# Kernel tuning notes

Hardware: AMD Instinct MI355X
Metric: run time of the kernel (lower is better)

Reference implementation:

```python
import jax, jax.numpy as jnp
import numpy as np

K = 20
BN_INV = float(1.0 / np.sqrt(1.0 + 1e-5))  # BatchNorm eval with running_mean=0, running_var=1


def _leaky(h):
    return jnp.where(h >= 0, h, 0.2 * h)


def _knn_idx(x, k):
    # x: [B, C, N]; pairwise_distance = -(||xi||^2 + ||xj||^2 - 2 xi.xj); topk = nearest
    inner = jnp.einsum('bcn,bcm->bnm', x, x)
    xx = jnp.sum(x * x, axis=1)  # [B, N]
    pd = 2.0 * inner - xx[:, :, None] - xx[:, None, :]
    return jax.lax.top_k(pd, k)[1]  # [B, N, k]


def _edge_conv(x, w, g, b, k):
    # x: [B, C, N]; w: [Cout, 2C]
    idx = _knn_idx(x, k)
    xt = jnp.transpose(x, (0, 2, 1))  # [B, N, C]
    nb = jax.vmap(lambda f, i: f[i])(xt, idx)  # [B, N, k, C] gathered neighbors
    ctr = xt[:, :, None, :]
    feat = jnp.concatenate([nb - ctr, jnp.broadcast_to(ctr, nb.shape)], axis=-1)  # [B,N,k,2C]
    h = jnp.einsum('bnkc,oc->bnko', feat, w)
    h = _leaky(g * h * BN_INV + b)
    h = jnp.max(h, axis=2)  # max over k neighbors -> [B, N, Cout]
    return jnp.transpose(h, (0, 2, 1))  # [B, Cout, N]


def setup_inputs() -> dict:
    key = jax.random.key(0)
    ks = jax.random.split(key, 32)
    s = 0.05

    def w(i, shape):
        return jax.random.normal(ks[i], shape, dtype=jnp.float32) * s

    def gb(i, c):
        return (1.0 + 0.1 * jax.random.normal(ks[i], (c,), dtype=jnp.float32),
                0.1 * jax.random.normal(jax.random.fold_in(ks[i], 1), (c,), dtype=jnp.float32))

    g1, b1 = gb(1, 64); g2, b2 = gb(2, 64); g3, b3 = gb(3, 128); g4, b4 = gb(4, 256)
    gc, bc = gb(5, 1024); gf1, bf1 = gb(6, 512); gf2, bf2 = gb(7, 256)
    return {
        'x': jax.random.normal(ks[0], (8, 3, 2048), dtype=jnp.float32),
        'w1': w(8, (64, 6)),   'g1': g1, 'b1': b1,
        'w2': w(9, (64, 128)), 'g2': g2, 'b2': b2,
        'w3': w(10, (128, 128)), 'g3': g3, 'b3': b3,
        'w4': w(11, (256, 256)), 'g4': g4, 'b4': b4,
        'wc': w(12, (1024, 512)), 'gc': gc, 'bc': bc,
        'wf1': w(13, (512, 2048)), 'gf1': gf1, 'bf1': bf1,
        'wf2': w(14, (256, 512)), 'bwf2': w(15, (256,)), 'gf2': gf2, 'bf2': bf2,
        'wf3': w(16, (40, 256)), 'bwf3': w(17, (40,)),
    }


def reference(x, w1, g1, b1, w2, g2, b2, w3, g3, b3, w4, g4, b4,
              wc, gc, bc, wf1, gf1, bf1, wf2, bwf2, gf2, bf2, wf3, bwf3):
    x1 = _edge_conv(x, w1, g1, b1, K)   # [B, 64, N]
    x2 = _edge_conv(x1, w2, g2, b2, K)  # [B, 64, N]
    x3 = _edge_conv(x2, w3, g3, b3, K)  # [B, 128, N]
    x4 = _edge_conv(x3, w4, g4, b4, K)  # [B, 256, N]
    h = jnp.concatenate([x1, x2, x3, x4], axis=1)  # [B, 512, N]
    h = jnp.einsum('bcn,oc->bon', h, wc)
    h = _leaky(gc[:, None] * h * BN_INV + bc[:, None])  # [B, 1024, N]
    x5 = jnp.max(h, axis=2)
    x6 = jnp.mean(h, axis=2)
    h = jnp.concatenate([x5, x6], axis=1)  # [B, 2048]
    h = _leaky(gf1 * (h @ wf1.T) * BN_INV + bf1)   # fc1 (no bias) + BN + LeakyReLU
    h = _leaky(gf2 * (h @ wf2.T + bwf2) * BN_INV + bf2)  # fc2 + BN + LeakyReLU (dropout=eval identity)
    return h @ wf3.T + bwf3  # [B, numClass]
```

## Files before the change

kernel.cpp:

```cpp
#include <hip/hip_runtime.h>
#include <hip/hip_bf16.h>
#include <float.h>

#define BB 8
#define NN 2048
#define KK 20

static constexpr float BN_INV_F = 0.9999950000374997f;

typedef __attribute__((ext_vector_type(4))) float f32x4;
typedef __attribute__((ext_vector_type(8))) short s16x8;

__device__ __forceinline__ unsigned short f2bf(float f) {
    __hip_bfloat16 h = __float2bfloat16(f);
    return __builtin_bit_cast(unsigned short, h);
}
__device__ __forceinline__ float bf2f(unsigned short u) {
    unsigned int v = ((unsigned int)u) << 16;
    return __builtin_bit_cast(float, v);
}
__device__ __forceinline__ unsigned mono(float f) {
    unsigned b = __builtin_bit_cast(unsigned, f);
    return b ^ (unsigned)(((int)b >> 31) | 0x80000000);
}

__global__ void split_kernel(const float* __restrict__ w, unsigned short* __restrict__ hi,
                             unsigned short* __restrict__ lo, int n) {
    int t = blockIdx.x * blockDim.x + threadIdx.x;
    if (t >= n) return;
    float v = w[t];
    unsigned short h = f2bf(v);
    hi[t] = h;
    lo[t] = f2bf(v - bf2f(h));
}

__global__ void sqnorm_kernel(const float* __restrict__ x, float* __restrict__ xx, int C) {
    int t = blockIdx.x * blockDim.x + threadIdx.x;
    if (t >= BB * NN) return;
    int b = t / NN, n = t % NN;
    const float* xb = x + (size_t)b * C * NN + n;
    float s = 0.f;
    for (int c = 0; c < C; ++c) {
        float v = xb[(size_t)c * NN];
        s += v * v;
    }
    xx[t] = s;
}

__global__ __launch_bounds__(256, 4) void pd_kernel(const float* __restrict__ x,
                                                    const float* __restrict__ xx,
                                                    float* __restrict__ pd,
                                                    int C, int baseB) {
    __shared__ float ctrT[128][8];
    __shared__ float xns[8];

    int blk = blockIdx.x;
    int chalf = blk & 1;
    int rt = (blk >> 1) & 255;
    int b2 = blk >> 9;
    int b = baseB + b2;
    int rbase = rt * 8;
    int tid = threadIdx.x;
    const float* xb = x + (size_t)b * C * NN;

    for (int i = tid; i < C * 8; i += 256) {
        int c = i >> 3, r = i & 7;
        ctrT[c][r] = xb[(size_t)c * NN + rbase + r];
    }
    if (tid < 8) xns[tid] = xx[b * NN + rbase + tid];
    __syncthreads();

    int m0 = chalf * 1024 + tid * 4;
    float acc[8][4];
    #pragma unroll
    for (int r = 0; r < 8; ++r)
        #pragma unroll
        for (int j = 0; j < 4; ++j) acc[r][j] = 0.f;

    f32x4 xv = *(const f32x4*)(xb + m0);
    for (int c = 0; c + 1 < C; ++c) {
        f32x4 nxt = *(const f32x4*)(xb + (size_t)(c + 1) * NN + m0);
        f32x4 c0 = *(const f32x4*)&ctrT[c][0];
        f32x4 c1 = *(const f32x4*)&ctrT[c][4];
        #pragma unroll
        for (int j = 0; j < 4; ++j) {
            acc[0][j] += c0.x * xv[j]; acc[1][j] += c0.y * xv[j];
            acc[2][j] += c0.z * xv[j]; acc[3][j] += c0.w * xv[j];
            acc[4][j] += c1.x * xv[j]; acc[5][j] += c1.y * xv[j];
            acc[6][j] += c1.z * xv[j]; acc[7][j] += c1.w * xv[j];
        }
        xv = nxt;
    }
    {
        f32x4 c0 = *(const f32x4*)&ctrT[C - 1][0];
        f32x4 c1 = *(const f32x4*)&ctrT[C - 1][4];
        #pragma unroll
        for (int j = 0; j < 4; ++j) {
            acc[0][j] += c0.x * xv[j]; acc[1][j] += c0.y * xv[j];
            acc[2][j] += c0.z * xv[j]; acc[3][j] += c0.w * xv[j];
            acc[4][j] += c1.x * xv[j]; acc[5][j] += c1.y * xv[j];
            acc[6][j] += c1.z * xv[j]; acc[7][j] += c1.w * xv[j];
        }
    }
    f32x4 xm = *(const f32x4*)(xx + (size_t)b * NN + m0);
    #pragma unroll
    for (int r = 0; r < 8; ++r) {
        f32x4 out;
        #pragma unroll
        for (int j = 0; j < 4; ++j)
            out[j] = 2.f * acc[r][j] - xns[r] - xm[j];
        *(f32x4*)&pd[((size_t)(b2 * NN + rbase + r)) * NN + m0] = out;
    }
}

__global__ __launch_bounds__(256, 4) void topk_kernel(const float* __restrict__ pd,
                                                      int* __restrict__ idxout, int baseB) {
    __shared__ unsigned long long cand[4][128];
    int w = threadIdx.x >> 6, lane = threadIdx.x & 63;
    int rowc = blockIdx.x * 4 + w;
    const float* prow = pd + (size_t)rowc * NN;

    float fv[32];
    #pragma unroll
    for (int j4 = 0; j4 < 8; ++j4) {
        f32x4 v = *(const f32x4*)(prow + j4 * 256 + lane * 4);
        #pragma unroll
        for (int e = 0; e < 4; ++e) fv[j4 * 4 + e] = v[e];
    }

    float lm = fv[0];
    #pragma unroll
    for (int i = 1; i < 32; ++i) lm = fmaxf(lm, fv[i]);

    float v = lm;
    #pragma unroll
    for (int k = 2; k <= 64; k <<= 1)
        #pragma unroll
        for (int j = k >> 1; j > 0; j >>= 1) {
            float o = __shfl_xor(v, j, 64);
            bool up = ((lane & k) == 0);
            bool keepMax = up ? ((lane & j) == 0) : ((lane & j) != 0);
            float mx = fmaxf(v, o), mn = fminf(v, o);
            v = keepMax ? mx : mn;
        }
    float Tf = __shfl(v, KK - 1, 64);

    cand[w][lane] = 0ull;
    cand[w][64 + lane] = 0ull;
    __builtin_amdgcn_wave_barrier();
    int base = 0;
    #pragma unroll
    for (int i = 0; i < 32; ++i) {
        int col = (i >> 2) * 256 + lane * 4 + (i & 3);
        bool c = fv[i] >= Tf;
        unsigned long long mask = __ballot(c);
        if (c) {
            int pos = base + (int)__popcll(mask & ((1ull << lane) - 1ull));
            if (pos < 128)
                cand[w][pos] = ((unsigned long long)mono(fv[i]) << 32) | (unsigned)~col;
        }
        base += (int)__popcll(mask);
    }
    __builtin_amdgcn_wave_barrier();

    unsigned long long ka = cand[w][lane];
    auto cmpx = [&](unsigned long long& key, int j, bool up) {
        unsigned long long o = __shfl_xor(key, j, 64);
        bool keepMax = up ? ((lane & j) == 0) : ((lane & j) != 0);
        bool gt = key > o;
        unsigned long long mx = gt ? key : o, mn = gt ? o : key;
        key = keepMax ? mx : mn;
    };
    if (base <= 64) {
        #pragma unroll
        for (int k = 2; k <= 64; k <<= 1)
            #pragma unroll
            for (int j = k >> 1; j > 0; j >>= 1)
                cmpx(ka, j, (lane & k) == 0);
    } else {
        unsigned long long kb = cand[w][64 + lane];
        #pragma unroll
        for (int k = 2; k <= 128; k <<= 1) {
            #pragma unroll
            for (int j = k >> 1; j > 0; j >>= 1) {
                if (j == 64) {
                    unsigned long long mx = ka > kb ? ka : kb;
                    unsigned long long mn = ka > kb ? kb : ka;
                    ka = mx; kb = mn;
                } else {
                    bool upA, upB;
                    if (k == 128)     { upA = true; upB = true; }
                    else if (k == 64) { upA = true; upB = false; }
                    else              { upA = ((lane & k) == 0); upB = upA; }
                    cmpx(ka, j, upA);
                    cmpx(kb, j, upB);
                }
            }
        }
    }

    if (lane < KK) {
        int col = (int)~(unsigned)(ka & 0xFFFFFFFFull);
        int b = baseB + (rowc >> 11);
        int n = rowc & 2047;
        idxout[((size_t)(b * NN + n)) * KK + lane] = col;
    }
}

__global__ __launch_bounds__(256) void pq_gemm_kernel(const float* __restrict__ x,
                                                      const float* __restrict__ w,
                                                      float* __restrict__ Pt, float* __restrict__ Qt,
                                                      int C, int Cout) {
    __shared__ float wPT[128][8];
    __shared__ float wQT[128][8];
    int blk = blockIdx.x;
    int pass = blk & 1;
    int rest = blk >> 1;
    int nog = Cout >> 3;
    int b = rest / nog;
    int obase = (rest % nog) * 8;
    int tid = threadIdx.x;
    const float* xb = x + (size_t)b * C * NN;

    for (int i = tid; i < C * 8; i += 256) {
        int c = i >> 3, r = i & 7;
        wPT[c][r] = w[(size_t)(obase + r) * 2 * C + c];
        wQT[c][r] = w[(size_t)(obase + r) * 2 * C + C + c];
    }
    __syncthreads();

    int m0 = pass * 1024 + tid * 4;
    float aP[8][4], aQ[8][4];
    #pragma unroll
    for (int r = 0; r < 8; ++r)
        #pragma unroll
        for (int j = 0; j < 4; ++j) { aP[r][j] = 0.f; aQ[r][j] = 0.f; }

    for (int c = 0; c < C; ++c) {
        f32x4 xv = *(const f32x4*)(xb + (size_t)c * NN + m0);
        f32x4 p0 = *(const f32x4*)&wPT[c][0];
        f32x4 p1 = *(const f32x4*)&wPT[c][4];
        f32x4 q0 = *(const f32x4*)&wQT[c][0];
        f32x4 q1 = *(const f32x4*)&wQT[c][4];
        #pragma unroll
        for (int j = 0; j < 4; ++j) {
            aP[0][j] += p0.x * xv[j]; aP[1][j] += p0.y * xv[j];
            aP[2][j] += p0.z * xv[j]; aP[3][j] += p0.w * xv[j];
            aP[4][j] += p1.x * xv[j]; aP[5][j] += p1.y * xv[j];
            aP[6][j] += p1.z * xv[j]; aP[7][j] += p1.w * xv[j];
            aQ[0][j] += q0.x * xv[j]; aQ[1][j] += q0.y * xv[j];
            aQ[2][j] += q0.z * xv[j]; aQ[3][j] += q0.w * xv[j];
            aQ[4][j] += q1.x * xv[j]; aQ[5][j] += q1.y * xv[j];
            aQ[6][j] += q1.z * xv[j]; aQ[7][j] += q1.w * xv[j];
        }
    }
    #pragma unroll
    for (int j = 0; j < 4; ++j) {
        size_t base = ((size_t)b * NN + m0 + j) * Cout + obase;
        f32x4 vP0, vP1, vQ0, vQ1;
        #pragma unroll
        for (int r = 0; r < 4; ++r) { vP0[r] = aP[r][j]; vP1[r] = aP[r + 4][j];
                                      vQ0[r] = aQ[r][j]; vQ1[r] = aQ[r + 4][j]; }
        *(f32x4*)&Pt[base] = vP0; *(f32x4*)&Pt[base + 4] = vP1;
        *(f32x4*)&Qt[base] = vQ0; *(f32x4*)&Qt[base + 4] = vQ1;
    }
}

__global__ __launch_bounds__(256) void edge_max_kernel(const float* __restrict__ Pt,
                                                       const float* __restrict__ Qt,
                                                       const int* __restrict__ idx,
                                                       const float* __restrict__ g,
                                                       const float* __restrict__ bt,
                                                       float* __restrict__ xf32,
                                                       unsigned short* __restrict__ Fhi,
                                                       unsigned short* __restrict__ Flo,
                                                       int coff, int Cout) {
    __shared__ int lidx[16][KK];
    int lanesPerN = Cout >> 2;
    int npw = 64 / lanesPerN;
    int nPerBlock = 4 * npw;

    int blk = blockIdx.x;
    int b = blk / (NN / nPerBlock);
    int nbase = (blk % (NN / nPerBlock)) * nPerBlock;
    int tid = threadIdx.x, wid = tid >> 6, lane = tid & 63;

    for (int i = tid; i < nPerBlock * KK; i += 256) {
        int ln = i / KK, k = i % KK;
        lidx[ln][k] = idx[((size_t)(b * NN + nbase + ln)) * KK + k];
    }
    __syncthreads();

    int nsub = lane / lanesPerN;
    int ol = (lane & (lanesPerN - 1)) * 4;
    int nrow = wid * npw + nsub;
    int n = nbase + nrow;

    const float* Pb = Pt + (size_t)b * NN * Cout;
    size_t rowbase = (size_t)n * Cout + ol;
    f32x4 Pn = *(const f32x4*)&Pb[rowbase];
    f32x4 Qn = *(const f32x4*)(Qt + (size_t)b * NN * Cout + rowbase);
    f32x4 off4 = Qn - Pn;
    f32x4 sc4 = *(const f32x4*)&g[ol];
    f32x4 bs4 = *(const f32x4*)&bt[ol];
    #pragma unroll
    for (int e = 0; e < 4; ++e) sc4[e] *= BN_INV_F;

    f32x4 mx4 = { -FLT_MAX, -FLT_MAX, -FLT_MAX, -FLT_MAX };
    #pragma unroll 4
    for (int k = 0; k < KK; ++k) {
        int m = lidx[nrow][k];
        f32x4 pv = *(const f32x4*)&Pb[(size_t)m * Cout + ol];
        #pragma unroll
        for (int e = 0; e < 4; ++e) {
            float y = sc4[e] * (pv[e] + off4[e]) + bs4[e];
            y = (y >= 0.f) ? y : 0.2f * y;
            mx4[e] = fmaxf(mx4[e], y);
        }
    }

    if (xf32) {
        #pragma unroll
        for (int e = 0; e < 4; ++e)
            xf32[((size_t)b * Cout + ol + e) * NN + n] = mx4[e];
    }
    size_t fb = ((size_t)b * NN + n) * 512 + coff + ol;
    ushort4 h4, l4;
    #pragma unroll
    for (int e = 0; e < 4; ++e) {
        unsigned short h = f2bf(mx4[e]);
        ((unsigned short*)&h4)[e] = h;
        ((unsigned short*)&l4)[e] = f2bf(mx4[e] - bf2f(h));
    }
    *(ushort4*)&Fhi[fb] = h4;
    *(ushort4*)&Flo[fb] = l4;
}

__global__ __launch_bounds__(256) void conv_mfma_kernel(const unsigned short* __restrict__ Whi,
                                                        const unsigned short* __restrict__ Wlo,
                                                        const unsigned short* __restrict__ Fhi,
                                                        const unsigned short* __restrict__ Flo,
                                                        const float* __restrict__ gc,
                                                        const float* __restrict__ bc,
                                                        float* __restrict__ pmax,
                                                        float* __restrict__ psum) {
    __shared__ unsigned short As[128 * 64] __attribute__((aligned(16)));
    __shared__ unsigned short Bs[128 * 64] __attribute__((aligned(16)));

    int blk = blockIdx.x;
    int nt = blk & 15, ot = (blk >> 4) & 7, b = blk >> 7;
    int obase = ot * 128, nbase = nt * 128;
    int tid = threadIdx.x, lane = tid & 63, wid = tid >> 6;
    int wo = wid >> 1, wn = wid & 1;

    f32x4 acc[4][4];
    #pragma unroll
    for (int m = 0; m < 4; ++m)
        #pragma unroll
        for (int q = 0; q < 4; ++q) acc[m][q] = (f32x4){0.f, 0.f, 0.f, 0.f};

    int srow = tid >> 1, sb = (tid & 1) * 4;

    for (int kt = 0; kt < 24; ++kt) {
        int seg = kt >> 3;
        int kc = (kt & 7) * 64;
        const unsigned short* Asrc = ((seg == 2) ? Wlo : Whi) + (size_t)obase * 512 + kc;
        const unsigned short* Bsrc = ((seg == 1) ? Flo : Fhi) + ((size_t)b * NN + nbase) * 512 + kc;
        __syncthreads();
        #pragma unroll
        for (int s = 0; s < 4; ++s) {
            int slot = sb + s;
            uint4 av = *(const uint4*)(Asrc + (size_t)srow * 512 + slot * 8);
            *(uint4*)(As + srow * 64 + ((slot ^ (srow & 7)) * 8)) = av;
            uint4 bv = *(const uint4*)(Bsrc + (size_t)srow * 512 + slot * 8);
            *(uint4*)(Bs + srow * 64 + ((slot ^ (srow & 7)) * 8)) = bv;
        }
        __syncthreads();
        #pragma unroll
        for (int ks = 0; ks < 2; ++ks) {
            s16x8 af[4], bf[4];
            #pragma unroll
            for (int m = 0; m < 4; ++m) {
                int r = wo * 64 + m * 16 + (lane & 15);
                int slot = (ks * 4 + (lane >> 4)) ^ (r & 7);
                af[m] = *(const s16x8*)(As + r * 64 + slot * 8);
                int r2 = wn * 64 + m * 16 + (lane & 15);
                int slot2 = (ks * 4 + (lane >> 4)) ^ (r2 & 7);
                bf[m] = *(const s16x8*)(Bs + r2 * 64 + slot2 * 8);
            }
            #pragma unroll
            for (int m = 0; m < 4; ++m)
                #pragma unroll
                for (int q = 0; q < 4; ++q)
                    acc[m][q] = __builtin_amdgcn_mfma_f32_16x16x32_bf16(af[m], bf[q], acc[m][q], 0, 0, 0);
        }
    }

    __syncthreads();
    float* redm = (float*)As;
    float* reds = redm + 256;
    #pragma unroll
    for (int m = 0; m < 4; ++m) {
        #pragma unroll
        for (int rg = 0; rg < 4; ++rg) {
            int olocal = wo * 64 + m * 16 + (lane >> 4) * 4 + rg;
            int o = obase + olocal;
            float scv = gc[o] * BN_INV_F, bsv = bc[o];
            float mx = -FLT_MAX, sm = 0.f;
            #pragma unroll
            for (int q = 0; q < 4; ++q) {
                float y = scv * acc[m][q][rg] + bsv;
                y = (y >= 0.f) ? y : 0.2f * y;
                mx = fmaxf(mx, y);
                sm += y;
            }
            #pragma unroll
            for (int d = 1; d < 16; d <<= 1) {
                mx = fmaxf(mx, __shfl_xor(mx, d, 64));
                sm += __shfl_xor(sm, d, 64);
            }
            if ((lane & 15) == 0) {
                redm[wn * 128 + olocal] = mx;
                reds[wn * 128 + olocal] = sm;
            }
        }
    }
    __syncthreads();
    if (tid < 128) {
        float mx = fmaxf(redm[tid], redm[128 + tid]);
        float sm = reds[tid] + reds[128 + tid];
        size_t base = ((size_t)b * 1024 + obase + tid) * 16 + nt;
        pmax[base] = mx;
        psum[base] = sm;
    }
}

__global__ void pool_reduce_kernel(const float* __restrict__ pmax, const float* __restrict__ psum,
                                   float* __restrict__ x56) {
    int t = blockIdx.x * blockDim.x + threadIdx.x;
    if (t >= BB * 1024) return;
    int b = t >> 10, o = t & 1023;
    float mx = -FLT_MAX, sm = 0.f;
    for (int ch = 0; ch < 16; ++ch) {
        mx = fmaxf(mx, pmax[(size_t)t * 16 + ch]);
        sm += psum[(size_t)t * 16 + ch];
    }
    x56[(size_t)b * 2048 + o] = mx;
    x56[(size_t)b * 2048 + 1024 + o] = sm * (1.0f / 2048.0f);
}

__global__ void fc_kernel(const float* __restrict__ in, const float* __restrict__ w,
                          const float* __restrict__ bw, const float* __restrict__ g,
                          const float* __restrict__ bt, float* __restrict__ out,
                          int Cin, int Cout, int mode) {
    int gt = blockIdx.x * blockDim.x + threadIdx.x;
    int wid = gt >> 6;
    int lane = threadIdx.x & 63;
    if (wid >= BB * Cout) return;
    int b = wid / Cout, o = wid % Cout;
    const float* ib = in + (size_t)b * Cin;
    const float* wr = w + (size_t)o * Cin;
    float acc = 0.f;
    for (int c = lane; c < Cin; c += 64) acc += ib[c] * wr[c];
    for (int d = 32; d >= 1; d >>= 1) acc += __shfl_down(acc, d, 64);
    if (lane == 0) {
        float y;
        if (mode == 0)      { y = g[o] * acc * BN_INV_F + bt[o]; y = (y >= 0.f) ? y : 0.2f * y; }
        else if (mode == 1) { float h = acc + bw[o]; y = g[o] * h * BN_INV_F + bt[o]; y = (y >= 0.f) ? y : 0.2f * y; }
        else                { y = acc + bw[o]; }
        out[(size_t)b * Cout + o] = y;
    }
}

extern "C" void kernel_launch(void* const* d_in, const int* in_sizes, int n_in,
                              void* d_out, int out_size, void* d_ws, size_t ws_size,
                              hipStream_t stream) {
    const float* x    = (const float*)d_in[0];
    const float* w1   = (const float*)d_in[1];
    const float* g1   = (const float*)d_in[2];
    const float* b1   = (const float*)d_in[3];
    const float* w2   = (const float*)d_in[4];
    const float* g2   = (const float*)d_in[5];
    const float* b2   = (const float*)d_in[6];
    const float* w3   = (const float*)d_in[7];
    const float* g3   = (const float*)d_in[8];
    const float* b3   = (const float*)d_in[9];
    const float* w4   = (const float*)d_in[10];
    const float* g4   = (const float*)d_in[11];
    const float* b4   = (const float*)d_in[12];
    const float* wc   = (const float*)d_in[13];
    const float* gc   = (const float*)d_in[14];
    const float* bc   = (const float*)d_in[15];
    const float* wf1  = (const float*)d_in[16];
    const float* gf1  = (const float*)d_in[17];
    const float* bf1  = (const float*)d_in[18];
    const float* wf2  = (const float*)d_in[19];
    const float* bwf2 = (const float*)d_in[20];
    const float* gf2  = (const float*)d_in[21];
    const float* bf2  = (const float*)d_in[22];
    const float* wf3  = (const float*)d_in[23];
    const float* bwf3 = (const float*)d_in[24];

    char* ws = (char*)d_ws;
    size_t off = 0;
    auto alloc = [&](size_t nbytes) {
        char* p = ws + off;
        off += (nbytes + 255) & ~(size_t)255;
        return p;
    };
    float* xx   = (float*)alloc((size_t)BB * NN * 4);
    int*   idx  = (int*)  alloc((size_t)BB * NN * KK * 4);
    float* Pt   = (float*)alloc((size_t)BB * NN * 256 * 4);
    float* Qt   = (float*)alloc((size_t)BB * NN * 256 * 4);
    float* x1   = (float*)alloc((size_t)BB * 64 * NN * 4);
    float* x2   = (float*)alloc((size_t)BB * 64 * NN * 4);
    float* x3   = (float*)alloc((size_t)BB * 128 * NN * 4);
    unsigned short* Fhi = (unsigned short*)alloc((size_t)BB * NN * 512 * 2);
    unsigned short* Flo = (unsigned short*)alloc((size_t)BB * NN * 512 * 2);
    unsigned short* Whi = (unsigned short*)alloc((size_t)1024 * 512 * 2);
    unsigned short* Wlo = (unsigned short*)alloc((size_t)1024 * 512 * 2);
    float* pmax = (float*)alloc((size_t)BB * 1024 * 16 * 4);
    float* psum = (float*)alloc((size_t)BB * 1024 * 16 * 4);
    float* x56  = (float*)alloc((size_t)BB * 2048 * 4);
    float* f1   = (float*)alloc((size_t)BB * 512 * 4);
    float* f2   = (float*)alloc((size_t)BB * 256 * 4);

    float* pdbuf = Pt;

    split_kernel<<<(1024 * 512 + 255) / 256, 256, 0, stream>>>(wc, Whi, Wlo, 1024 * 512);

    struct Layer { const float* xin; int C; const float* w; const float* g; const float* bt;
                   float* xout; int Cout; int coff; };
    Layer L[4] = {
        { x,  3,   w1, g1, b1, x1,      64,  0   },
        { x1, 64,  w2, g2, b2, x2,      64,  64  },
        { x2, 64,  w3, g3, b3, x3,      128, 128 },
        { x3, 128, w4, g4, b4, nullptr, 256, 256 },
    };

    for (int l = 0; l < 4; ++l) {
        sqnorm_kernel<<<(BB * NN) / 256, 256, 0, stream>>>(L[l].xin, xx, L[l].C);
        for (int ch = 0; ch < 4; ++ch) {
            pd_kernel<<<1024, 256, 0, stream>>>(L[l].xin, xx, pdbuf, L[l].C, ch * 2);
            topk_kernel<<<1024, 256, 0, stream>>>(pdbuf, idx, ch * 2);
        }
        pq_gemm_kernel<<<BB * (L[l].Cout / 8) * 2, 256, 0, stream>>>(L[l].xin, L[l].w, Pt, Qt, L[l].C, L[l].Cout);
        int nPerBlock = 4 * (64 / (L[l].Cout >> 2));
        edge_max_kernel<<<BB * (NN / nPerBlock), 256, 0, stream>>>(Pt, Qt, idx, L[l].g, L[l].bt,
                                                                   L[l].xout, Fhi, Flo, L[l].coff, L[l].Cout);
    }

    conv_mfma_kernel<<<BB * 8 * 16, 256, 0, stream>>>(Whi, Wlo, Fhi, Flo, gc, bc, pmax, psum);
    pool_reduce_kernel<<<(BB * 1024 + 255) / 256, 256, 0, stream>>>(pmax, psum, x56);
    fc_kernel<<<(BB * 512 * 64 + 255) / 256, 256, 0, stream>>>(x56, wf1, nullptr, gf1, bf1, f1, 2048, 512, 0);
    fc_kernel<<<(BB * 256 * 64 + 255) / 256, 256, 0, stream>>>(f1, wf2, bwf2, gf2, bf2, f2, 512, 256, 1);
    fc_kernel<<<(BB * 40 * 64 + 255) / 256, 256, 0, stream>>>(f2, wf3, bwf3, nullptr, nullptr, (float*)d_out, 256, 40, 2);
}
```

Measured before the change: 849.9 us.

## Fuse pairwise-distance and top-k into one kernel using shared-memory rows

Replaces the chunked pd_kernel + topk_kernel pairs with a single kernel per layer that computes the distance rows for 4 points at a time into LDS and then selects the top-k directly from shared memory. This removes the global write and re-read of the full distance matrix and cuts eight launches per layer down to one. In exchange, each block handles 8 rows in two batches of 4 with extra syncthreads. It also needs about 36KB of LDS per block, which may limit occupancy, and the smaller 4-row register tile re-reads x for each batch.

```diff
diff --git a/kernel.cpp b/kernel.cpp
--- a/kernel.cpp
+++ b/kernel.cpp
@@ -47,163 +47,163 @@
     xx[t] = s;
 }
 
-__global__ __launch_bounds__(256, 4) void pd_kernel(const float* __restrict__ x,
-                                                    const float* __restrict__ xx,
-                                                    float* __restrict__ pd,
-                                                    int C, int baseB) {
-    __shared__ float ctrT[128][8];
+__global__ __launch_bounds__(256, 4) void knn_fused_kernel(const float* __restrict__ x,
+                                                           const float* __restrict__ xx,
+                                                           int* __restrict__ idxout, int C) {
+    __shared__ float pdl[4][NN];
+    __shared__ char ubuf[4096];
     __shared__ float xns[8];
 
+    float* ctrT = (float*)ubuf;
+    unsigned long long (*cand)[128] = (unsigned long long (*)[128])ubuf;
+
     int blk = blockIdx.x;
-    int chalf = blk & 1;
-    int rt = (blk >> 1) & 255;
-    int b2 = blk >> 9;
-    int b = baseB + b2;
-    int rbase = rt * 8;
+    int b = blk / (NN / 8);
+    int rbase = (blk % (NN / 8)) * 8;
     int tid = threadIdx.x;
     const float* xb = x + (size_t)b * C * NN;
 
-    for (int i = tid; i < C * 8; i += 256) {
-        int c = i >> 3, r = i & 7;
-        ctrT[c][r] = xb[(size_t)c * NN + rbase + r];
-    }
     if (tid < 8) xns[tid] = xx[b * NN + rbase + tid];
-    __syncthreads();
-
-    int m0 = chalf * 1024 + tid * 4;
-    float acc[8][4];
-    #pragma unroll
-    for (int r = 0; r < 8; ++r)
-        #pragma unroll
-        for (int j = 0; j < 4; ++j) acc[r][j] = 0.f;
-
-    f32x4 xv = *(const f32x4*)(xb + m0);
-    for (int c = 0; c + 1 < C; ++c) {
-        f32x4 nxt = *(const f32x4*)(xb + (size_t)(c + 1) * NN + m0);
-        f32x4 c0 = *(const f32x4*)&ctrT[c][0];
-        f32x4 c1 = *(const f32x4*)&ctrT[c][4];
-        #pragma unroll
-        for (int j = 0; j < 4; ++j) {
-            acc[0][j] += c0.x * xv[j]; acc[1][j] += c0.y * xv[j];
-            acc[2][j] += c0.z * xv[j]; acc[3][j] += c0.w * xv[j];
-            acc[4][j] += c1.x * xv[j]; acc[5][j] += c1.y * xv[j];
-            acc[6][j] += c1.z * xv[j]; acc[7][j] += c1.w * xv[j];
-        }
-        xv = nxt;
-    }
-    {
-        f32x4 c0 = *(const f32x4*)&ctrT[C - 1][0];
-        f32x4 c1 = *(const f32x4*)&ctrT[C - 1][4];
-        #pragma unroll
-        for (int j = 0; j < 4; ++j) {
-            acc[0][j] += c0.x * xv[j]; acc[1][j] += c0.y * xv[j];
-            acc[2][j] += c0.z * xv[j]; acc[3][j] += c0.w * xv[j];
-            acc[4][j] += c1.x * xv[j]; acc[5][j] += c1.y * xv[j];
-            acc[6][j] += c1.z * xv[j]; acc[7][j] += c1.w * xv[j];
-        }
-    }
-    f32x4 xm = *(const f32x4*)(xx + (size_t)b * NN + m0);
-    #pragma unroll
-    for (int r = 0; r < 8; ++r) {
-        f32x4 out;
-        #pragma unroll
-        for (int j = 0; j < 4; ++j)
-            out[j] = 2.f * acc[r][j] - xns[r] - xm[j];
-        *(f32x4*)&pd[((size_t)(b2 * NN + rbase + r)) * NN + m0] = out;
-    }
-}
-
-__global__ __launch_bounds__(256, 4) void topk_kernel(const float* __restrict__ pd,
-                                                      int* __restrict__ idxout, int baseB) {
-    __shared__ unsigned long long cand[4][128];
-    int w = threadIdx.x >> 6, lane = threadIdx.x & 63;
-    int rowc = blockIdx.x * 4 + w;
-    const float* prow = pd + (size_t)rowc * NN;
-
-    float fv[32];
-    #pragma unroll
-    for (int j4 = 0; j4 < 8; ++j4) {
-        f32x4 v = *(const f32x4*)(prow + j4 * 256 + lane * 4);
-        #pragma unroll
-        for (int e = 0; e < 4; ++e) fv[j4 * 4 + e] = v[e];
-    }
-
-    float lm = fv[0];
-    #pragma unroll
-    for (int i = 1; i < 32; ++i) lm = fmaxf(lm, fv[i]);
-
-    float v = lm;
-    #pragma unroll
-    for (int k = 2; k <= 64; k <<= 1)
-        #pragma unroll
-        for (int j = k >> 1; j > 0; j >>= 1) {
-            float o = __shfl_xor(v, j, 64);
-            bool up = ((lane & k) == 0);
-            bool keepMax = up ? ((lane & j) == 0) : ((lane & j) != 0);
-            float mx = fmaxf(v, o), mn = fminf(v, o);
-            v = keepMax ? mx : mn;
-        }
-    float Tf = __shfl(v, KK - 1, 64);
-
-    cand[w][lane] = 0ull;
-    cand[w][64 + lane] = 0ull;
-    __builtin_amdgcn_wave_barrier();
-    int base = 0;
-    #pragma unroll
-    for (int i = 0; i < 32; ++i) {
-        int col = (i >> 2) * 256 + lane * 4 + (i & 3);
-        bool c = fv[i] >= Tf;
-        unsigned long long mask = __ballot(c);
-        if (c) {
-            int pos = base + (int)__popcll(mask & ((1ull << lane) - 1ull));
-            if (pos < 128)
-                cand[w][pos] = ((unsigned long long)mono(fv[i]) << 32) | (unsigned)~col;
-        }
-        base += (int)__popcll(mask);
-    }
-    __builtin_amdgcn_wave_barrier();
-
-    unsigned long long ka = cand[w][lane];
-    auto cmpx = [&](unsigned long long& key, int j, bool up) {
-        unsigned long long o = __shfl_xor(key, j, 64);
-        bool keepMax = up ? ((lane & j) == 0) : ((lane & j) != 0);
-        bool gt = key > o;
-        unsigned long long mx = gt ? key : o, mn = gt ? o : key;
-        key = keepMax ? mx : mn;
-    };
-    if (base <= 64) {
-        #pragma unroll
-        for (int k = 2; k <= 64; k <<= 1)
-            #pragma unroll
-            for (int j = k >> 1; j > 0; j >>= 1)
-                cmpx(ka, j, (lane & k) == 0);
-    } else {
-        unsigned long long kb = cand[w][64 + lane];
-        #pragma unroll
-        for (int k = 2; k <= 128; k <<= 1) {
-            #pragma unroll
-            for (int j = k >> 1; j > 0; j >>= 1) {
-                if (j == 64) {
-                    unsigned long long mx = ka > kb ? ka : kb;
-                    unsigned long long mn = ka > kb ? kb : ka;
-                    ka = mx; kb = mn;
-                } else {
-                    bool upA, upB;
-                    if (k == 128)     { upA = true; upB = true; }
-                    else if (k == 64) { upA = true; upB = false; }
-                    else              { upA = ((lane & k) == 0); upB = upA; }
-                    cmpx(ka, j, upA);
-                    cmpx(kb, j, upB);
+
+    int w = tid >> 6, lane = tid & 63;
+
+    for (int bat = 0; bat < 2; ++bat) {
+        __syncthreads();
+        for (int i = tid; i < C * 4; i += 256) {
+            int c = i >> 2, r = i & 3;
+            ctrT[c * 4 + r] = xb[(size_t)c * NN + rbase + bat * 4 + r];
+        }
+        __syncthreads();
+
+        for (int pass = 0; pass < 2; ++pass) {
+            int m0 = pass * 1024 + tid * 4;
+            float acc[4][4];
+            #pragma unroll
+            for (int r = 0; r < 4; ++r)
+                #pragma unroll
+                for (int j = 0; j < 4; ++j) acc[r][j] = 0.f;
+
+            f32x4 xv = *(const f32x4*)(xb + m0);
+            for (int c = 0; c + 1 < C; ++c) {
+                f32x4 nxt = *(const f32x4*)(xb + (size_t)(c + 1) * NN + m0);
+                f32x4 c0 = *(const f32x4*)&ctrT[c * 4];
+                #pragma unroll
+                for (int j = 0; j < 4; ++j) {
+                    acc[0][j] += c0.x * xv[j];
+                    acc[1][j] += c0.y * xv[j];
+                    acc[2][j] += c0.z * xv[j];
+                    acc[3][j] += c0.w * xv[j];
                 }
-            }
-        }
-    }
-
-    if (lane < KK) {
-        int col = (int)~(unsigned)(ka & 0xFFFFFFFFull);
-        int b = baseB + (rowc >> 11);
-        int n = rowc & 2047;
-        idxout[((size_t)(b * NN + n)) * KK + lane] = col;
+                xv = nxt;
+            }
+            {
+                f32x4 c0 = *(const f32x4*)&ctrT[(C - 1) * 4];
+                #pragma unroll
+                for (int j = 0; j < 4; ++j) {
+                    acc[0][j] += c0.x * xv[j];
+                    acc[1][j] += c0.y * xv[j];
+                    acc[2][j] += c0.z * xv[j];
+                    acc[3][j] += c0.w * xv[j];
+                }
+            }
+            f32x4 xm = *(const f32x4*)(xx + (size_t)b * NN + m0);
+            #pragma unroll
+            for (int r = 0; r < 4; ++r) {
+                f32x4 out;
+                #pragma unroll
+                for (int j = 0; j < 4; ++j)
+                    out[j] = 2.f * acc[r][j] - xns[bat * 4 + r] - xm[j];
+                *(f32x4*)&pdl[r][m0] = out;
+            }
+        }
+        __syncthreads();
+
+        {
+            const float* prow = pdl[w];
+            float fv[32];
+            #pragma unroll
+            for (int j4 = 0; j4 < 8; ++j4) {
+                f32x4 v = *(const f32x4*)&prow[j4 * 256 + lane * 4];
+                #pragma unroll
+                for (int e = 0; e < 4; ++e) fv[j4 * 4 + e] = v[e];
+            }
+
+            float lm = fv[0];
+            #pragma unroll
+            for (int i = 1; i < 32; ++i) lm = fmaxf(lm, fv[i]);
+
+            float v = lm;
+            #pragma unroll
+            for (int k = 2; k <= 64; k <<= 1)
+                #pragma unroll
+                for (int j = k >> 1; j > 0; j >>= 1) {
+                    float o = __shfl_xor(v, j, 64);
+                    bool up = ((lane & k) == 0);
+                    bool keepMax = up ? ((lane & j) == 0) : ((lane & j) != 0);
+                    float mx = fmaxf(v, o), mn = fminf(v, o);
+                    v = keepMax ? mx : mn;
+                }
+            float Tf = __shfl(v, KK - 1, 64);
+
+            cand[w][lane] = 0ull;
+            cand[w][64 + lane] = 0ull;
+            __builtin_amdgcn_wave_barrier();
+            int base = 0;
+            #pragma unroll
+            for (int i = 0; i < 32; ++i) {
+                int col = (i >> 2) * 256 + lane * 4 + (i & 3);
+                bool c = fv[i] >= Tf;
+                unsigned long long mask = __ballot(c);
+                if (c) {
+                    int pos = base + (int)__popcll(mask & ((1ull << lane) - 1ull));
+                    if (pos < 128)
+                        cand[w][pos] = ((unsigned long long)mono(fv[i]) << 32) | (unsigned)~col;
+                }
+                base += (int)__popcll(mask);
+            }
+            __builtin_amdgcn_wave_barrier();
+
+            unsigned long long ka = cand[w][lane];
+            auto cmpx = [&](unsigned long long& key, int j, bool up) {
+                unsigned long long o = __shfl_xor(key, j, 64);
+                bool keepMax = up ? ((lane & j) == 0) : ((lane & j) != 0);
+                bool gt = key > o;
+                unsigned long long mx = gt ? key : o, mn = gt ? o : key;
+                key = keepMax ? mx : mn;
+            };
+            if (base <= 64) {
+                #pragma unroll
+                for (int k = 2; k <= 64; k <<= 1)
+                    #pragma unroll
+                    for (int j = k >> 1; j > 0; j >>= 1)
+                        cmpx(ka, j, (lane & k) == 0);
+            } else {
+                unsigned long long kb = cand[w][64 + lane];
+                #pragma unroll
+                for (int k = 2; k <= 128; k <<= 1) {
+                    #pragma unroll
+                    for (int j = k >> 1; j > 0; j >>= 1) {
+                        if (j == 64) {
+                            unsigned long long mx = ka > kb ? ka : kb;
+                            unsigned long long mn = ka > kb ? kb : ka;
+                            ka = mx; kb = mn;
+                        } else {
+                            bool upA, upB;
+                            if (k == 128)     { upA = true; upB = true; }
+                            else if (k == 64) { upA = true; upB = false; }
+                            else              { upA = ((lane & k) == 0); upB = upA; }
+                            cmpx(ka, j, upA);
+                            cmpx(kb, j, upB);
+                        }
+                    }
+                }
+            }
+
+            if (lane < KK) {
+                int col = (int)~(unsigned)(ka & 0xFFFFFFFFull);
+                idxout[((size_t)(b * NN + rbase + bat * 4 + w)) * KK + lane] = col;
+            }
+        }
     }
 }
 
@@ -525,8 +525,6 @@
     float* f1   = (float*)alloc((size_t)BB * 512 * 4);
     float* f2   = (float*)alloc((size_t)BB * 256 * 4);
 
-    float* pdbuf = Pt;
-
     split_kernel<<<(1024 * 512 + 255) / 256, 256, 0, stream>>>(wc, Whi, Wlo, 1024 * 512);
 
     struct Layer { const float* xin; int C; const float* w; const float* g; const float* bt;
@@ -540,10 +538,7 @@
 
     for (int l = 0; l < 4; ++l) {
         sqnorm_kernel<<<(BB * NN) / 256, 256, 0, stream>>>(L[l].xin, xx, L[l].C);
-        for (int ch = 0; ch < 4; ++ch) {
-            pd_kernel<<<1024, 256, 0, stream>>>(L[l].xin, xx, pdbuf, L[l].C, ch * 2);
-            topk_kernel<<<1024, 256, 0, stream>>>(pdbuf, idx, ch * 2);
-        }
+        knn_fused_kernel<<<BB * (NN / 8), 256, 0, stream>>>(L[l].xin, xx, idx, L[l].C);
         pq_gemm_kernel<<<BB * (L[l].Cout / 8) * 2, 256, 0, stream>>>(L[l].xin, L[l].w, Pt, Qt, L[l].C, L[l].Cout);
         int nPerBlock = 4 * (64 / (L[l].Cout >> 2));
         edge_max_kernel<<<BB * (NN / nPerBlock), 256, 0, stream>>>(Pt, Qt, idx, L[l].g, L[l].bt,
```

Result: slower. 897.1 us (+5.6%).
